# Performance work log

Measured on AMD Instinct MI355X. Metric: run time of the kernel, lower is better.

Reference implementation:

```python
import jax, jax.numpy as jnp
import numpy as np

B, S, D, E, H, K = 2, 2048, 1024, 8, 4096, 2


def setup_inputs() -> dict:
    key = jax.random.key(0)
    ks = jax.random.split(key, 7)
    sd = 1.0 / np.sqrt(D)
    sh = 1.0 / np.sqrt(H)
    return {
        "x": jax.random.normal(ks[0], (B, S, D), dtype=jnp.float32),
        "router_w": jax.random.uniform(ks[1], (D, E), jnp.float32, -sd, sd),
        "router_b": jnp.zeros((E,), jnp.float32),
        "w1": jax.random.uniform(ks[2], (E, D, H), jnp.float32, -sd, sd),
        "b1": jnp.zeros((E, H), jnp.float32),
        "w2": jax.random.uniform(ks[3], (E, H, D), jnp.float32, -sh, sh),
        "b2": jnp.zeros((E, D), jnp.float32),
    }


def reference(x, router_w, router_b, w1, b1, w2, b2):
    # Router: softmax over experts, then top-k and renormalize
    router_logits = jnp.einsum("bsd,de->bse", x, router_w) + router_b
    router_probs = jax.nn.softmax(router_logits, axis=-1)
    top_k_probs, top_k_indices = jax.lax.top_k(router_probs, K)  # [B,S,K]
    top_k_probs = top_k_probs / jnp.sum(top_k_probs, axis=-1, keepdims=True)

    # Dense all-expert FFN (Block assumed: Linear -> GELU -> Linear)
    h = jax.nn.gelu(jnp.einsum("bsd,edh->bseh", x, w1) + b1)  # [B,S,E,H]
    expert_outputs = jnp.einsum("bseh,ehd->bsed", h, w2) + b2  # [B,S,E,D]

    # Gather top-k experts per token and combine with renormalized probs
    idx = top_k_indices[..., None]  # [B,S,K,1]
    selected = jnp.take_along_axis(expert_outputs, idx, axis=2)  # [B,S,K,D]
    return jnp.sum(selected * top_k_probs[..., None], axis=2)  # [B,S,D]
```

## Files before the change

kernel.cpp:

```cpp
#include <hip/hip_runtime.h>
#include <hip/hip_bf16.h>

#define TOK   4096
#define DDIM  1024
#define NEXP  8
#define HDIM  4096
#define KSEL  2
#define NPAIR (TOK * KSEL)
#define NSPLIT 4
#define MAXT  72

typedef __attribute__((ext_vector_type(8))) _Float16 f16x8;
typedef __attribute__((ext_vector_type(4))) _Float16 f16x4;
typedef __attribute__((ext_vector_type(4))) float    f32x4;

__device__ __forceinline__ void gload16(const void* g, void* l) {
  __builtin_amdgcn_global_load_lds((const __attribute__((address_space(1))) void*)g,
                                   (__attribute__((address_space(3))) void*)l, 16, 0, 0);
}

__device__ __forceinline__ float gelu_tanh(float u) {
  float inner = 0.7978845608028654f * (u + 0.044715f * u * u * u);
  float t2 = __expf(2.f * inner);
  return u - u / (t2 + 1.f);
}

__global__ __launch_bounds__(256) void k_router(const float* __restrict__ x,
    const float* __restrict__ rw, const float* __restrict__ rb,
    int* __restrict__ tidx, float* __restrict__ tw,
    _Float16* __restrict__ xb) {
  const int t    = blockIdx.x * 4 + (threadIdx.x >> 6);
  const int lane = threadIdx.x & 63;
  const float* xr = x + (size_t)t * DDIM;
  _Float16*   xbr = xb + (size_t)t * DDIM;
  float acc[NEXP];
#pragma unroll
  for (int e = 0; e < NEXP; ++e) acc[e] = 0.f;
  for (int d0 = lane * 4; d0 < DDIM; d0 += 256) {
    const float4 xv = *(const float4*)(xr + d0);
    f16x4 hx;
    hx[0] = (_Float16)xv.x; hx[1] = (_Float16)xv.y;
    hx[2] = (_Float16)xv.z; hx[3] = (_Float16)xv.w;
    *(f16x4*)(xbr + d0) = hx;
#pragma unroll
    for (int i = 0; i < 4; ++i) {
      const float xs = (&xv.x)[i];
      const float4 r0 = *(const float4*)(rw + (size_t)(d0 + i) * NEXP);
      const float4 r1 = *(const float4*)(rw + (size_t)(d0 + i) * NEXP + 4);
      acc[0] += xs * r0.x; acc[1] += xs * r0.y; acc[2] += xs * r0.z; acc[3] += xs * r0.w;
      acc[4] += xs * r1.x; acc[5] += xs * r1.y; acc[6] += xs * r1.z; acc[7] += xs * r1.w;
    }
  }
#pragma unroll
  for (int e = 0; e < NEXP; ++e) {
    float v = acc[e];
#pragma unroll
    for (int s = 32; s; s >>= 1) v += __shfl_xor(v, s, 64);
    acc[e] = v;
  }
  if (lane == 0) {
    float lg[NEXP];
#pragma unroll
    for (int e = 0; e < NEXP; ++e) lg[e] = acc[e] + rb[e];
    int i0 = 0;
#pragma unroll
    for (int e = 1; e < NEXP; ++e) if (lg[e] > lg[i0]) i0 = e;
    int i1 = -1; float best = -3.4e38f;
#pragma unroll
    for (int e = 0; e < NEXP; ++e) {
      if (e == i0) continue;
      if (lg[e] > best) { best = lg[e]; i1 = e; }
    }
    float w0 = 1.f / (1.f + expf(lg[i1] - lg[i0]));
    tidx[t * 2]     = i0;  tidx[t * 2 + 1] = i1;
    tw[t * 2]       = w0;  tw[t * 2 + 1]   = 1.f - w0;
  }
}

__global__ __launch_bounds__(1024) void k_scan(const int* __restrict__ tidx,
                       const float* __restrict__ tw,
                       int* __restrict__ offs,
                       int* __restrict__ row_token, float* __restrict__ row_w,
                       int* __restrict__ inv,
                       int* __restrict__ tlist, int* __restrict__ tcount) {
  __shared__ int hist[NEXP];
  __shared__ int soff[NEXP + 1];
  __shared__ int scur[NEXP];
  if (threadIdx.x < NEXP) hist[threadIdx.x] = 0;
  __syncthreads();
  const int lane = threadIdx.x & 63;
  int e_loc[NPAIR / 1024];
#pragma unroll
  for (int it = 0; it < NPAIR / 1024; ++it) {
    const int p = it * 1024 + threadIdx.x;
    const int e = tidx[p];
    e_loc[it] = e;
#pragma unroll
    for (int ee = 0; ee < NEXP; ++ee) {
      unsigned long long m = __ballot(e == ee);
      if (m && lane == 0) atomicAdd(&hist[ee], __popcll(m));
    }
  }
  __syncthreads();
  if (threadIdx.x == 0) {
    int run = 0;
    for (int e = 0; e < NEXP; ++e) { soff[e] = run; scur[e] = run; run += hist[e]; }
    soff[NEXP] = run;
    for (int e = 0; e <= NEXP; ++e) offs[e] = soff[e];
    int cnt = 0;
    for (int e = 0; e < NEXP; ++e) {
      const int ne = soff[e + 1] - soff[e];
      for (int m = 0; m < ne; m += 128) tlist[cnt++] = (e << 8) | (m >> 7);
    }
    *tcount = cnt;
  }
  __syncthreads();
#pragma unroll
  for (int it = 0; it < NPAIR / 1024; ++it) {
    const int p = it * 1024 + threadIdx.x;
    const int e = e_loc[it];
    int pos = 0;
#pragma unroll
    for (int ee = 0; ee < NEXP; ++ee) {
      unsigned long long m = __ballot(e == ee);
      if (!m) continue;
      int base = 0;
      if (lane == 0) base = atomicAdd(&scur[ee], __popcll(m));
      base = __shfl(base, 0, 64);
      if (e == ee) pos = base + __popcll(m & ((1ull << lane) - 1ull));
    }
    row_token[pos] = p >> 1;
    row_w[pos]     = tw[p];
    inv[p]         = pos;
  }
}

__global__ __launch_bounds__(256) void k_transpose2(const float* __restrict__ w1,
    const float* __restrict__ w2, _Float16* __restrict__ w1t, _Float16* __restrict__ w2t) {
  __shared__ _Float16 tile[64][72];
  const int zz = blockIdx.y;
  const float* ip; _Float16* op; int Rr, Cc, i0, j0;
  if (zz < NEXP) {
    ip = w1 + (size_t)zz * DDIM * HDIM;  op = w1t + (size_t)zz * DDIM * HDIM;
    Rr = DDIM; Cc = HDIM;
    i0 = (blockIdx.x >> 6) * 64; j0 = (blockIdx.x & 63) * 64;
  } else {
    ip = w2 + (size_t)(zz - NEXP) * HDIM * DDIM;  op = w2t + (size_t)(zz - NEXP) * HDIM * DDIM;
    Rr = HDIM; Cc = DDIM;
    i0 = (blockIdx.x >> 4) * 64; j0 = (blockIdx.x & 15) * 64;
  }
  const int tx = threadIdx.x & 15, ty = threadIdx.x >> 4;
#pragma unroll
  for (int rr = 0; rr < 4; ++rr) {
    int r = ty + rr * 16;
    float4 v = *(const float4*)(ip + (size_t)(i0 + r) * Cc + j0 + tx * 4);
    tile[r][tx * 4 + 0] = (_Float16)v.x;
    tile[r][tx * 4 + 1] = (_Float16)v.y;
    tile[r][tx * 4 + 2] = (_Float16)v.z;
    tile[r][tx * 4 + 3] = (_Float16)v.w;
  }
  __syncthreads();
#pragma unroll
  for (int cc = 0; cc < 4; ++cc) {
    int c = ty + cc * 16;
    f16x4 o;
#pragma unroll
    for (int k = 0; k < 4; ++k) o[k] = tile[tx * 4 + k][c];
    *(f16x4*)(op + (size_t)(j0 + c) * Rr + i0 + tx * 4) = o;
  }
}

#define BM 128
#define BN 128
#define BKK 32


__global__ __launch_bounds__(256) void k_gemm1(
    const _Float16* __restrict__ xb,
    const _Float16* __restrict__ w1t,
    const float* __restrict__ b1,
    const int* __restrict__ offs,
    const int* __restrict__ row_token,
    const int* __restrict__ tlist, const int* __restrict__ tcount,
    _Float16* __restrict__ hbuf) {
  const int bid = blockIdx.x;
  const int t   = bid >> 5;
  if (t >= *tcount) return;
  const int tl  = tlist[t];
  const int e   = tl >> 8;
  const int m0  = (tl & 255) * BM;
  const int n0  = (bid & 31) * BN;
  const int off0 = offs[e];
  const int ne   = offs[e + 1] - off0;
  const int mrem = ne - m0;

  __shared__ __align__(16) char smem[32768];

  const int tid = threadIdx.x;
  const int wv = tid >> 6, lane = tid & 63;
  const int l15 = lane & 15;
  const int wr = wv >> 1, wc = wv & 1;

  const int rA0 = (wv * 2 + 0) * 16 + (lane >> 2);
  const int rA1 = (wv * 2 + 1) * 16 + (lane >> 2);
  const char* a_c = (const char*)xb;
  const char* b_c = (const char*)(w1t + (size_t)e * HDIM * DDIM);
  const int rc0 = (rA0 < mrem) ? rA0 : (mrem - 1);
  const int rc1 = (rA1 < mrem) ? rA1 : (mrem - 1);
  const char* ap0 = a_c + (size_t)row_token[off0 + m0 + rc0] * (DDIM * 2)
                        + (((lane & 3) ^ ((rA0 >> 1) & 3)) << 4);
  const char* ap1 = a_c + (size_t)row_token[off0 + m0 + rc1] * (DDIM * 2)
                        + (((lane & 3) ^ ((rA1 >> 1) & 3)) << 4);
  const char* bp0 = b_c + (size_t)(n0 + rA0) * (DDIM * 2)
                        + (((lane & 3) ^ ((rA0 >> 1) & 3)) << 4);
  const char* bp1 = b_c + (size_t)(n0 + rA1) * (DDIM * 2)
                        + (((lane & 3) ^ ((rA1 >> 1) & 3)) << 4);
  char* ldsA0 = smem + (wv * 2 + 0) * 1024;
  char* ldsA1 = smem + (wv * 2 + 1) * 1024;
  char* ldsB0 = smem + 16384 + (wv * 2 + 0) * 1024;
  char* ldsB1 = smem + 16384 + (wv * 2 + 1) * 1024;

  const unsigned foff = (unsigned)(((lane >> 4) ^ ((l15 >> 1) & 3)) << 4);

  f32x4 acc[4][4] = {};
  const int NT = DDIM / BKK;

  gload16(ap0, ldsA0); gload16(ap1, ldsA1);
  gload16(bp0, ldsB0); gload16(bp1, ldsB1);

#pragma unroll 2
  for (int ks = 0; ks < NT; ++ks) {
    const int cur = ks & 1;
    if (ks + 1 < NT) {
      const int nb = (cur ^ 1) * 8192;
      const size_t kb = (size_t)(ks + 1) * 64;
      gload16(ap0 + kb, ldsA0 + nb); gload16(ap1 + kb, ldsA1 + nb);
      gload16(bp0 + kb, ldsB0 + nb); gload16(bp1 + kb, ldsB1 + nb);
      asm volatile("s_waitcnt vmcnt(4)" ::: "memory");
    } else {
      asm volatile("s_waitcnt vmcnt(0)" ::: "memory");
    }
    __builtin_amdgcn_sched_barrier(0);
    __builtin_amdgcn_s_barrier();
    const char* Ab = smem + cur * 8192;
    const char* Bb = smem + 16384 + cur * 8192;
    f16x8 af[4], bfr[4];
#pragma unroll
    for (int m = 0; m < 4; ++m)
      af[m] = *(const f16x8*)(Ab + (wr * 64 + m * 16 + l15) * 64 + foff);
#pragma unroll
    for (int n = 0; n < 4; ++n)
      bfr[n] = *(const f16x8*)(Bb + (wc * 64 + n * 16 + l15) * 64 + foff);
#pragma unroll
    for (int m = 0; m < 4; ++m)
#pragma unroll
      for (int n = 0; n < 4; ++n)
        acc[m][n] = __builtin_amdgcn_mfma_f32_16x16x32_f16(af[m], bfr[n], acc[m][n], 0, 0, 0);
    __builtin_amdgcn_sched_barrier(0);
    __builtin_amdgcn_s_barrier();
  }

  float bias[4];
#pragma unroll
  for (int n = 0; n < 4; ++n)
    bias[n] = b1[(size_t)e * HDIM + n0 + wc * 64 + n * 16 + l15];
#pragma unroll
  for (int m = 0; m < 4; ++m) {
#pragma unroll
    for (int j = 0; j < 4; ++j) {
      int row = wr * 64 + m * 16 + (lane >> 4) * 4 + j;
#pragma unroll
      for (int n = 0; n < 4; ++n) {
        int col = wc * 64 + n * 16 + l15;
        *(_Float16*)(smem + (row << 8) + (((col << 1) ^ ((row & 15) << 4)))) =
            (_Float16)gelu_tanh(acc[m][n][j] + bias[n]);
      }
    }
  }
  __syncthreads();
  {
    const int srow = tid >> 1, half = tid & 1;
    if (srow < mrem) {
      _Float16* hr = hbuf + (size_t)(off0 + m0 + srow) * HDIM + n0 + half * 64;
#pragma unroll
      for (int i = 0; i < 8; ++i) {
        f16x8 v = *(const f16x8*)(smem + (srow << 8) + (((half * 128 + i * 16) ^ ((srow & 15) << 4))));
        *(f16x8*)(hr + i * 8) = v;
      }
    }
  }
}

__global__ __launch_bounds__(256) void k_gemm2(
    const _Float16* __restrict__ hbuf,
    const _Float16* __restrict__ w2t,
    const int* __restrict__ offs,
    const int* __restrict__ tlist, const int* __restrict__ tcount,
    _Float16* __restrict__ yb) {
  const int bid = blockIdx.x;
  const int t   = bid >> 5;
  if (t >= *tcount) return;
  const int tl  = tlist[t];
  const int e   = tl >> 8;
  const int m0  = (tl & 255) * BM;
  const int sub = bid & 31;
  const int kh  = sub >> 3;
  const int n0  = (sub & 7) * BN;
  const int off0 = offs[e];
  const int ne   = offs[e + 1] - off0;
  const int mrem = ne - m0;

  __shared__ __align__(16) char smem[32768];

  const int tid = threadIdx.x;
  const int wv = tid >> 6, lane = tid & 63;
  const int l15 = lane & 15;
  const int wr = wv >> 1, wc = wv & 1;

  const int rA0 = (wv * 2 + 0) * 16 + (lane >> 2);
  const int rA1 = (wv * 2 + 1) * 16 + (lane >> 2);
  const char* a_c = (const char*)hbuf;
  const char* b_c = (const char*)(w2t + (size_t)e * DDIM * HDIM);
  const int rc0 = (rA0 < mrem) ? rA0 : (mrem - 1);
  const int rc1 = (rA1 < mrem) ? rA1 : (mrem - 1);
  const size_t khb = (size_t)kh * ((HDIM / NSPLIT) * 2);
  const char* ap0 = a_c + (size_t)(off0 + m0 + rc0) * (HDIM * 2) + khb
                        + (((lane & 3) ^ ((rA0 >> 1) & 3)) << 4);
  const char* ap1 = a_c + (size_t)(off0 + m0 + rc1) * (HDIM * 2) + khb
                        + (((lane & 3) ^ ((rA1 >> 1) & 3)) << 4);
  const char* bp0 = b_c + (size_t)(n0 + rA0) * (HDIM * 2) + khb
                        + (((lane & 3) ^ ((rA0 >> 1) & 3)) << 4);
  const char* bp1 = b_c + (size_t)(n0 + rA1) * (HDIM * 2) + khb
                        + (((lane & 3) ^ ((rA1 >> 1) & 3)) << 4);
  char* ldsA0 = smem + (wv * 2 + 0) * 1024;
  char* ldsA1 = smem + (wv * 2 + 1) * 1024;
  char* ldsB0 = smem + 16384 + (wv * 2 + 0) * 1024;
  char* ldsB1 = smem + 16384 + (wv * 2 + 1) * 1024;

  const unsigned foff = (unsigned)(((lane >> 4) ^ ((l15 >> 1) & 3)) << 4);

  f32x4 acc[4][4] = {};
  const int NT = (HDIM / NSPLIT) / BKK;

  gload16(ap0, ldsA0); gload16(ap1, ldsA1);
  gload16(bp0, ldsB0); gload16(bp1, ldsB1);

#pragma unroll 2
  for (int ks = 0; ks < NT; ++ks) {
    const int cur = ks & 1;
    if (ks + 1 < NT) {
      const int nb = (cur ^ 1) * 8192;
      const size_t kb = (size_t)(ks + 1) * 64;
      gload16(ap0 + kb, ldsA0 + nb); gload16(ap1 + kb, ldsA1 + nb);
      gload16(bp0 + kb, ldsB0 + nb); gload16(bp1 + kb, ldsB1 + nb);
      asm volatile("s_waitcnt vmcnt(4)" ::: "memory");
    } else {
      asm volatile("s_waitcnt vmcnt(0)" ::: "memory");
    }
    __builtin_amdgcn_sched_barrier(0);
    __builtin_amdgcn_s_barrier();
    const char* Ab = smem + cur * 8192;
    const char* Bb = smem + 16384 + cur * 8192;
    f16x8 af[4], bfr[4];
#pragma unroll
    for (int m = 0; m < 4; ++m)
      af[m] = *(const f16x8*)(Ab + (wr * 64 + m * 16 + l15) * 64 + foff);
#pragma unroll
    for (int n = 0; n < 4; ++n)
      bfr[n] = *(const f16x8*)(Bb + (wc * 64 + n * 16 + l15) * 64 + foff);
#pragma unroll
    for (int m = 0; m < 4; ++m)
#pragma unroll
      for (int n = 0; n < 4; ++n)
        acc[m][n] = __builtin_amdgcn_mfma_f32_16x16x32_f16(af[m], bfr[n], acc[m][n], 0, 0, 0);
    __builtin_amdgcn_sched_barrier(0);
    __builtin_amdgcn_s_barrier();
  }

  _Float16* ypart = yb + (size_t)kh * NPAIR * DDIM;
#pragma unroll
  for (int m = 0; m < 4; ++m) {
#pragma unroll
    for (int j = 0; j < 4; ++j) {
      int row = wr * 64 + m * 16 + (lane >> 4) * 4 + j;
#pragma unroll
      for (int n = 0; n < 4; ++n) {
        int col = wc * 64 + n * 16 + l15;
        *(_Float16*)(smem + (row << 8) + (((col << 1) ^ ((row & 15) << 4)))) =
            (_Float16)acc[m][n][j];
      }
    }
  }
  __syncthreads();
  {
    const int srow = tid >> 1, half = tid & 1;
    if (srow < mrem) {
      _Float16* yr = ypart + (size_t)(off0 + m0 + srow) * DDIM + n0 + half * 64;
#pragma unroll
      for (int i = 0; i < 8; ++i) {
        f16x8 v = *(const f16x8*)(smem + (srow << 8) + (((half * 128 + i * 16) ^ ((srow & 15) << 4))));
        *(f16x8*)(yr + i * 8) = v;
      }
    }
  }
}

__global__ __launch_bounds__(256) void k_combine(const _Float16* __restrict__ yb,
    const int* __restrict__ inv, const int* __restrict__ tidx,
    const float* __restrict__ tw, const float* __restrict__ b2,
    float* __restrict__ out) {
  const int t  = blockIdx.x * 2 + (threadIdx.x >> 7);
  const int c8 = (threadIdx.x & 127) * 8;
  const int g0 = inv[2 * t],  g1 = inv[2 * t + 1];
  const int e0 = tidx[2 * t], e1 = tidx[2 * t + 1];
  const float w0 = tw[2 * t], w1 = tw[2 * t + 1];
  float s0[8] = {0,0,0,0,0,0,0,0}, s1[8] = {0,0,0,0,0,0,0,0};
#pragma unroll
  for (int p = 0; p < NSPLIT; ++p) {
    const _Float16* yp = yb + (size_t)p * NPAIR * DDIM;
    f16x8 a = *(const f16x8*)(yp + (size_t)g0 * DDIM + c8);
    f16x8 b = *(const f16x8*)(yp + (size_t)g1 * DDIM + c8);
#pragma unroll
    for (int i = 0; i < 8; ++i) { s0[i] += (float)a[i]; s1[i] += (float)b[i]; }
  }
  float o[8];
#pragma unroll
  for (int i = 0; i < 8; ++i) {
    float bA = b2[(size_t)e0 * DDIM + c8 + i];
    float bB = b2[(size_t)e1 * DDIM + c8 + i];
    o[i] = w0 * (s0[i] + bA) + w1 * (s1[i] + bB);
  }
  float* op = out + (size_t)t * DDIM + c8;
  *(float4*)op       = make_float4(o[0], o[1], o[2], o[3]);
  *(float4*)(op + 4) = make_float4(o[4], o[5], o[6], o[7]);
}

extern "C" void kernel_launch(void* const* d_in, const int* in_sizes, int n_in,
                              void* d_out, int out_size, void* d_ws, size_t ws_size,
                              hipStream_t stream) {
  const float* x  = (const float*)d_in[0];
  const float* rw = (const float*)d_in[1];
  const float* rb = (const float*)d_in[2];
  const float* w1 = (const float*)d_in[3];
  const float* b1 = (const float*)d_in[4];
  const float* w2 = (const float*)d_in[5];
  const float* b2 = (const float*)d_in[6];
  float* out = (float*)d_out;
  char* ws = (char*)d_ws;

  int*      tidx    = (int*)(ws + 0);
  float*    tw      = (float*)(ws + 32768);
  int*      tcount  = (int*)(ws + 65536);
  int*      tlist   = (int*)(ws + 65544);
  int*      offs    = (int*)(ws + 65856);
  int*      row_tok = (int*)(ws + 66048);
  float*    row_w   = (float*)(ws + 98816);
  int*      inv     = (int*)(ws + 131584);
  _Float16* xb      = (_Float16*)(ws + 164352);
  _Float16* wtA     = (_Float16*)(ws + 8552960);
  _Float16* wtB     = (_Float16*)(ws + 75661824);
  _Float16* hb      = (_Float16*)(ws + 142770688);
  _Float16* yb      = wtA;

  k_router<<<dim3(TOK / 4), 256, 0, stream>>>(x, rw, rb, tidx, tw, xb);
  k_scan<<<dim3(1), 1024, 0, stream>>>(tidx, tw, offs, row_tok, row_w, inv, tlist, tcount);
  k_transpose2<<<dim3(1024, 2 * NEXP), 256, 0, stream>>>(w1, w2, wtA, wtB);
  k_gemm1<<<dim3(MAXT * 32), 256, 0, stream>>>(xb, wtA, b1, offs, row_tok, tlist, tcount, hb);
  k_gemm2<<<dim3(MAXT * 32), 256, 0, stream>>>(hb, wtB, offs, tlist, tcount, yb);
  k_combine<<<dim3(TOK / 2), 256, 0, stream>>>(yb, inv, tidx, tw, b2, out);
}
```

Measured before the change: 356.0 us.

## Fuse router with weight transpose, halve GEMM2 split-K, widen transpose stores

Folds the router and the fp32-to-fp16 weight transpose into one launch, which removes a kernel boundary and lets router blocks overlap with transpose blocks. The transpose now uses a 66-wide LDS tile and writes two 16-byte vectors per thread instead of 8-byte ones, aiming for better global write coalescing. GEMM2's split-K factor drops from 4 to 2, which halves the partial-output traffic that the combine kernel must read. The cost is fewer GEMM2 blocks, with a longer K loop per block and less parallelism.

```diff
diff --git a/kernel.cpp b/kernel.cpp
--- a/kernel.cpp
+++ b/kernel.cpp
@@ -7,7 +7,7 @@
 #define HDIM  4096
 #define KSEL  2
 #define NPAIR (TOK * KSEL)
-#define NSPLIT 4
+#define NSPLIT 2
 #define MAXT  72
 
 typedef __attribute__((ext_vector_type(8))) _Float16 f16x8;
@@ -25,55 +25,94 @@
   return u - u / (t2 + 1.f);
 }
 
-__global__ __launch_bounds__(256) void k_router(const float* __restrict__ x,
+__global__ __launch_bounds__(256) void k_prep(const float* __restrict__ x,
     const float* __restrict__ rw, const float* __restrict__ rb,
-    int* __restrict__ tidx, float* __restrict__ tw,
-    _Float16* __restrict__ xb) {
-  const int t    = blockIdx.x * 4 + (threadIdx.x >> 6);
-  const int lane = threadIdx.x & 63;
-  const float* xr = x + (size_t)t * DDIM;
-  _Float16*   xbr = xb + (size_t)t * DDIM;
-  float acc[NEXP];
-#pragma unroll
-  for (int e = 0; e < NEXP; ++e) acc[e] = 0.f;
-  for (int d0 = lane * 4; d0 < DDIM; d0 += 256) {
-    const float4 xv = *(const float4*)(xr + d0);
-    f16x4 hx;
-    hx[0] = (_Float16)xv.x; hx[1] = (_Float16)xv.y;
-    hx[2] = (_Float16)xv.z; hx[3] = (_Float16)xv.w;
-    *(f16x4*)(xbr + d0) = hx;
-#pragma unroll
-    for (int i = 0; i < 4; ++i) {
-      const float xs = (&xv.x)[i];
-      const float4 r0 = *(const float4*)(rw + (size_t)(d0 + i) * NEXP);
-      const float4 r1 = *(const float4*)(rw + (size_t)(d0 + i) * NEXP + 4);
-      acc[0] += xs * r0.x; acc[1] += xs * r0.y; acc[2] += xs * r0.z; acc[3] += xs * r0.w;
-      acc[4] += xs * r1.x; acc[5] += xs * r1.y; acc[6] += xs * r1.z; acc[7] += xs * r1.w;
-    }
-  }
-#pragma unroll
-  for (int e = 0; e < NEXP; ++e) {
-    float v = acc[e];
-#pragma unroll
-    for (int s = 32; s; s >>= 1) v += __shfl_xor(v, s, 64);
-    acc[e] = v;
-  }
-  if (lane == 0) {
-    float lg[NEXP];
-#pragma unroll
-    for (int e = 0; e < NEXP; ++e) lg[e] = acc[e] + rb[e];
-    int i0 = 0;
-#pragma unroll
-    for (int e = 1; e < NEXP; ++e) if (lg[e] > lg[i0]) i0 = e;
-    int i1 = -1; float best = -3.4e38f;
+    const float* __restrict__ w1, const float* __restrict__ w2,
+    int* __restrict__ tidx, float* __restrict__ tw, _Float16* __restrict__ xb,
+    _Float16* __restrict__ w1t, _Float16* __restrict__ w2t) {
+  if (blockIdx.x < 1024) {
+    const int t    = blockIdx.x * 4 + (threadIdx.x >> 6);
+    const int lane = threadIdx.x & 63;
+    const float* xr = x + (size_t)t * DDIM;
+    _Float16*   xbr = xb + (size_t)t * DDIM;
+    float acc[NEXP];
+#pragma unroll
+    for (int e = 0; e < NEXP; ++e) acc[e] = 0.f;
+    for (int d0 = lane * 4; d0 < DDIM; d0 += 256) {
+      const float4 xv = *(const float4*)(xr + d0);
+      f16x4 hx;
+      hx[0] = (_Float16)xv.x; hx[1] = (_Float16)xv.y;
+      hx[2] = (_Float16)xv.z; hx[3] = (_Float16)xv.w;
+      *(f16x4*)(xbr + d0) = hx;
+#pragma unroll
+      for (int i = 0; i < 4; ++i) {
+        const float xs = (&xv.x)[i];
+        const float4 r0 = *(const float4*)(rw + (size_t)(d0 + i) * NEXP);
+        const float4 r1 = *(const float4*)(rw + (size_t)(d0 + i) * NEXP + 4);
+        acc[0] += xs * r0.x; acc[1] += xs * r0.y; acc[2] += xs * r0.z; acc[3] += xs * r0.w;
+        acc[4] += xs * r1.x; acc[5] += xs * r1.y; acc[6] += xs * r1.z; acc[7] += xs * r1.w;
+      }
+    }
 #pragma unroll
     for (int e = 0; e < NEXP; ++e) {
-      if (e == i0) continue;
-      if (lg[e] > best) { best = lg[e]; i1 = e; }
-    }
-    float w0 = 1.f / (1.f + expf(lg[i1] - lg[i0]));
-    tidx[t * 2]     = i0;  tidx[t * 2 + 1] = i1;
-    tw[t * 2]       = w0;  tw[t * 2 + 1]   = 1.f - w0;
+      float v = acc[e];
+#pragma unroll
+      for (int s = 32; s; s >>= 1) v += __shfl_xor(v, s, 64);
+      acc[e] = v;
+    }
+    if (lane == 0) {
+      float lg[NEXP];
+#pragma unroll
+      for (int e = 0; e < NEXP; ++e) lg[e] = acc[e] + rb[e];
+      int i0 = 0;
+#pragma unroll
+      for (int e = 1; e < NEXP; ++e) if (lg[e] > lg[i0]) i0 = e;
+      int i1 = -1; float best = -3.4e38f;
+#pragma unroll
+      for (int e = 0; e < NEXP; ++e) {
+        if (e == i0) continue;
+        if (lg[e] > best) { best = lg[e]; i1 = e; }
+      }
+      float w0 = 1.f / (1.f + expf(lg[i1] - lg[i0]));
+      tidx[t * 2]     = i0;  tidx[t * 2 + 1] = i1;
+      tw[t * 2]       = w0;  tw[t * 2 + 1]   = 1.f - w0;
+    }
+    return;
+  }
+  __shared__ _Float16 tile[64][66];
+  const int bx = blockIdx.x - 1024;
+  const int zz = bx >> 10;
+  const int xx = bx & 1023;
+  const float* ip; _Float16* op; int Rr, Cc, i0, j0;
+  if (zz < NEXP) {
+    ip = w1 + (size_t)zz * DDIM * HDIM;  op = w1t + (size_t)zz * DDIM * HDIM;
+    Rr = DDIM; Cc = HDIM;
+    i0 = (xx >> 6) * 64; j0 = (xx & 63) * 64;
+  } else {
+    ip = w2 + (size_t)(zz - NEXP) * HDIM * DDIM;  op = w2t + (size_t)(zz - NEXP) * HDIM * DDIM;
+    Rr = HDIM; Cc = DDIM;
+    i0 = (xx >> 4) * 64; j0 = (xx & 15) * 64;
+  }
+  const int tx = threadIdx.x & 15, ty = threadIdx.x >> 4;
+#pragma unroll
+  for (int rr = 0; rr < 4; ++rr) {
+    int r = ty + rr * 16;
+    float4 v = *(const float4*)(ip + (size_t)(i0 + r) * Cc + j0 + tx * 4);
+    tile[r][tx * 4 + 0] = (_Float16)v.x;
+    tile[r][tx * 4 + 1] = (_Float16)v.y;
+    tile[r][tx * 4 + 2] = (_Float16)v.z;
+    tile[r][tx * 4 + 3] = (_Float16)v.w;
+  }
+  __syncthreads();
+  {
+    const int c  = threadIdx.x >> 2;
+    const int s0 = (threadIdx.x & 3) * 16;
+    f16x8 v0, v1;
+#pragma unroll
+    for (int k = 0; k < 8; ++k) { v0[k] = tile[s0 + k][c]; v1[k] = tile[s0 + 8 + k][c]; }
+    _Float16* outp = op + (size_t)(j0 + c) * Rr + i0 + s0;
+    *(f16x8*)outp       = v0;
+    *(f16x8*)(outp + 8) = v1;
   }
 }
 
@@ -132,41 +171,6 @@
     row_token[pos] = p >> 1;
     row_w[pos]     = tw[p];
     inv[p]         = pos;
-  }
-}
-
-__global__ __launch_bounds__(256) void k_transpose2(const float* __restrict__ w1,
-    const float* __restrict__ w2, _Float16* __restrict__ w1t, _Float16* __restrict__ w2t) {
-  __shared__ _Float16 tile[64][72];
-  const int zz = blockIdx.y;
-  const float* ip; _Float16* op; int Rr, Cc, i0, j0;
-  if (zz < NEXP) {
-    ip = w1 + (size_t)zz * DDIM * HDIM;  op = w1t + (size_t)zz * DDIM * HDIM;
-    Rr = DDIM; Cc = HDIM;
-    i0 = (blockIdx.x >> 6) * 64; j0 = (blockIdx.x & 63) * 64;
-  } else {
-    ip = w2 + (size_t)(zz - NEXP) * HDIM * DDIM;  op = w2t + (size_t)(zz - NEXP) * HDIM * DDIM;
-    Rr = HDIM; Cc = DDIM;
-    i0 = (blockIdx.x >> 4) * 64; j0 = (blockIdx.x & 15) * 64;
-  }
-  const int tx = threadIdx.x & 15, ty = threadIdx.x >> 4;
-#pragma unroll
-  for (int rr = 0; rr < 4; ++rr) {
-    int r = ty + rr * 16;
-    float4 v = *(const float4*)(ip + (size_t)(i0 + r) * Cc + j0 + tx * 4);
-    tile[r][tx * 4 + 0] = (_Float16)v.x;
-    tile[r][tx * 4 + 1] = (_Float16)v.y;
-    tile[r][tx * 4 + 2] = (_Float16)v.z;
-    tile[r][tx * 4 + 3] = (_Float16)v.w;
-  }
-  __syncthreads();
-#pragma unroll
-  for (int cc = 0; cc < 4; ++cc) {
-    int c = ty + cc * 16;
-    f16x4 o;
-#pragma unroll
-    for (int k = 0; k < 4; ++k) o[k] = tile[tx * 4 + k][c];
-    *(f16x4*)(op + (size_t)(j0 + c) * Rr + i0 + tx * 4) = o;
   }
 }
 
@@ -298,12 +302,12 @@
     const int* __restrict__ tlist, const int* __restrict__ tcount,
     _Float16* __restrict__ yb) {
   const int bid = blockIdx.x;
-  const int t   = bid >> 5;
+  const int t   = bid >> 4;
   if (t >= *tcount) return;
   const int tl  = tlist[t];
   const int e   = tl >> 8;
   const int m0  = (tl & 255) * BM;
-  const int sub = bid & 31;
+  const int sub = bid & 15;
   const int kh  = sub >> 3;
   const int n0  = (sub & 7) * BN;
   const int off0 = offs[e];
@@ -414,21 +418,17 @@
   const int g0 = inv[2 * t],  g1 = inv[2 * t + 1];
   const int e0 = tidx[2 * t], e1 = tidx[2 * t + 1];
   const float w0 = tw[2 * t], w1 = tw[2 * t + 1];
-  float s0[8] = {0,0,0,0,0,0,0,0}, s1[8] = {0,0,0,0,0,0,0,0};
-#pragma unroll
-  for (int p = 0; p < NSPLIT; ++p) {
-    const _Float16* yp = yb + (size_t)p * NPAIR * DDIM;
-    f16x8 a = *(const f16x8*)(yp + (size_t)g0 * DDIM + c8);
-    f16x8 b = *(const f16x8*)(yp + (size_t)g1 * DDIM + c8);
-#pragma unroll
-    for (int i = 0; i < 8; ++i) { s0[i] += (float)a[i]; s1[i] += (float)b[i]; }
-  }
+  const _Float16* y1p = yb + (size_t)NPAIR * DDIM;
+  f16x8 a0 = *(const f16x8*)(yb  + (size_t)g0 * DDIM + c8);
+  f16x8 a1 = *(const f16x8*)(y1p + (size_t)g0 * DDIM + c8);
+  f16x8 b0 = *(const f16x8*)(yb  + (size_t)g1 * DDIM + c8);
+  f16x8 b1v = *(const f16x8*)(y1p + (size_t)g1 * DDIM + c8);
   float o[8];
 #pragma unroll
   for (int i = 0; i < 8; ++i) {
     float bA = b2[(size_t)e0 * DDIM + c8 + i];
     float bB = b2[(size_t)e1 * DDIM + c8 + i];
-    o[i] = w0 * (s0[i] + bA) + w1 * (s1[i] + bB);
+    o[i] = w0 * ((float)a0[i] + (float)a1[i] + bA) + w1 * ((float)b0[i] + (float)b1v[i] + bB);
   }
   float* op = out + (size_t)t * DDIM + c8;
   *(float4*)op       = make_float4(o[0], o[1], o[2], o[3]);
@@ -462,10 +462,10 @@
   _Float16* hb      = (_Float16*)(ws + 142770688);
   _Float16* yb      = wtA;
 
-  k_router<<<dim3(TOK / 4), 256, 0, stream>>>(x, rw, rb, tidx, tw, xb);
+  k_prep<<<dim3(1024 + 16 * 1024), 256, 0, stream>>>(x, rw, rb, w1, w2,
+                                                     tidx, tw, xb, wtA, wtB);
   k_scan<<<dim3(1), 1024, 0, stream>>>(tidx, tw, offs, row_tok, row_w, inv, tlist, tcount);
-  k_transpose2<<<dim3(1024, 2 * NEXP), 256, 0, stream>>>(w1, w2, wtA, wtB);
   k_gemm1<<<dim3(MAXT * 32), 256, 0, stream>>>(xb, wtA, b1, offs, row_tok, tlist, tcount, hb);
-  k_gemm2<<<dim3(MAXT * 32), 256, 0, stream>>>(hb, wtB, offs, tlist, tcount, yb);
+  k_gemm2<<<dim3(MAXT * 16), 256, 0, stream>>>(hb, wtB, offs, tlist, tcount, yb);
   k_combine<<<dim3(TOK / 2), 256, 0, stream>>>(yb, inv, tidx, tw, b2, out);
 }
```

After: 346.1 us (median of 3 runs). 2.8% less time.
